# Optimization experiments

Measured on AMD Instinct MI355X. Metric: run time of the kernel, lower is better.

## Reference

```python
import jax, jax.numpy as jnp
import numpy as np

D = 1024      # d_model
E = 8         # num_experts
K = 2         # top_k
H = 4096      # expert_dim (bottleneck)
P = 256       # proj_dim
BATCH, SEQ = 2, 2048
CLAMP_MAX = float(np.log(1.0 / 0.01))
INIT_T = 0.5


def setup_inputs() -> dict:
    key = jax.random.key(0)
    ks = jax.random.split(key, 6)
    x = jax.random.normal(ks[0], (BATCH, SEQ, D), jnp.float32)
    # cosine projector (nn.Linear default init ~ U(-1/sqrt(D), 1/sqrt(D)))
    lim = 1.0 / np.sqrt(D)
    Wp = jax.random.uniform(ks[1], (P, D), jnp.float32, -lim, lim)
    bp = jnp.zeros((P,), jnp.float32)
    sim = 0.01 * jax.random.normal(ks[2], (P, E), jnp.float32)
    temp = jnp.full((1,), np.log(1.0 / INIT_T), jnp.float32)
    # RepAdapter 1x1 convs == linear layers; xavier_uniform, zero bias
    bA = float(np.sqrt(6.0 / (D + H)))
    A = jax.random.uniform(ks[3], (E, H, D), jnp.float32, -bA, bA)
    a_bias = jnp.zeros((E, H), jnp.float32)
    Bw = jax.random.uniform(ks[4], (E, D, H), jnp.float32, -bA, bA)
    b_bias = jnp.zeros((E, D), jnp.float32)
    return dict(x=x, Wp=Wp, bp=bp, sim=sim, temp=temp, A=A, a_bias=a_bias, Bw=Bw, b_bias=b_bias)


def reference(x, Wp, bp, sim, temp, A, a_bias, Bw, b_bias):
    B, S, d = x.shape
    e = sim.shape[1]
    xf = x.reshape(-1, d)                                  # [T, D]
    # cosine gate
    proj = xf @ Wp.T + bp                                  # [T, P]
    projn = proj / jnp.maximum(jnp.linalg.norm(proj, axis=1, keepdims=True), 1e-12)
    simn = sim / jnp.maximum(jnp.linalg.norm(sim, axis=0, keepdims=True), 1e-12)
    scale = jnp.exp(jnp.minimum(temp, CLAMP_MAX))          # [1]
    gate_probs = jax.nn.softmax((projn @ simn) * scale, axis=-1)   # [T, E]
    topv, topi = jax.lax.top_k(gate_probs, K)              # [T, K]
    topv = topv / (topv.sum(axis=-1, keepdims=True) + 1e-8)
    # per-token per-expert combine weight
    w = jnp.sum(topv[:, :, None] * jax.nn.one_hot(topi, e, dtype=x.dtype), axis=1)  # [T, E]

    # experts: y_e(x) = x + B_e(A_e x + a_e) + b_e (no nonlinearity); combine weighted
    def body(acc, params):
        Ae, ab, Be, bb, we = params
        h = xf @ Ae.T + ab                                 # [T, H]
        f = h @ Be.T + bb                                  # [T, D]
        return acc + we[:, None] * (xf + f), None

    out, _ = jax.lax.scan(body, jnp.zeros_like(xf), (A, a_bias, Bw, b_bias, w.T))
    out = out.reshape(B, S, d)

    frac = gate_probs.mean(axis=0)                         # expert_fractions
    aux_loss = jnp.sum((frac - 1.0 / e) ** 2)
    usage = jnp.bincount(topi.reshape(-1), length=e).astype(jnp.float32)
    return out, aux_loss, frac, usage
```

## Files before the change

kernel.cpp:

```cpp
#include <hip/hip_runtime.h>
#include <stdint.h>


typedef __attribute__((ext_vector_type(4))) float floatx4;
typedef __attribute__((ext_vector_type(8))) short shortx8;
typedef unsigned short ushort_t;

#define T_TOKENS 4096
#define D_DIM    1024
#define E_EXP    8
#define H_DIM    4096
#define P_DIM    256
#define ROWS_PAD 9344
#define MBLK     73

__device__ __forceinline__ ushort_t f2bf(float f) {
  union { float f; unsigned int u; } c; c.f = f;
  unsigned int u = c.u;
  unsigned int r = u + 0x7FFFu + ((u >> 16) & 1u);
  return (ushort_t)(r >> 16);
}

__global__ __launch_bounds__(256) void k_cvt(const float* __restrict__ src,
                                             ushort_t* __restrict__ dst, int n4) {
  int g = blockIdx.x * 256 + threadIdx.x;
  if (g >= n4) return;
  floatx4 v = ((const floatx4*)src)[g];
  ushort4 o; o.x = f2bf(v.x); o.y = f2bf(v.y); o.z = f2bf(v.z); o.w = f2bf(v.w);
  ((ushort4*)dst)[g] = o;
}

__global__ __launch_bounds__(256) void k_small_init(int* counts, int* cursor,
                                                    float* frac_sum, int* row2tok) {
  int g = blockIdx.x * 256 + threadIdx.x;
  if (g < 8) { counts[g] = 0; cursor[g] = 0; frac_sum[g] = 0.f; }
  if (g < ROWS_PAD) row2tok[g] = -1;
}

__global__ __launch_bounds__(256) void k_proj(const float* __restrict__ x,
                                              const float* __restrict__ Wp,
                                              const float* __restrict__ bp,
                                              float* __restrict__ proj) {
  __shared__ float Wc[256 * 36];
  __shared__ float Xc[16 * 36];
  int tid = threadIdx.x;
  int t0 = blockIdx.x * 16;
  int cg = tid & 31, tg = tid >> 5;
  floatx4 acc[2][8];
#pragma unroll
  for (int a = 0; a < 2; a++)
#pragma unroll
    for (int b = 0; b < 8; b++) acc[a][b] = (floatx4){0.f, 0.f, 0.f, 0.f};
  for (int kc = 0; kc < 32; ++kc) {
    int k0 = kc * 32;
    __syncthreads();
#pragma unroll
    for (int it = 0; it < 8; ++it) {
      int f = it * 256 + tid;
      int j = f >> 3, kk = (f & 7) << 2;
      floatx4 v = *(const floatx4*)(Wp + j * 1024 + k0 + kk);
      *(floatx4*)(Wc + j * 36 + kk) = v;
    }
    if (tid < 128) {
      int t = tid >> 3, kk = (tid & 7) << 2;
      floatx4 v = *(const floatx4*)(x + (size_t)(t0 + t) * 1024 + k0 + kk);
      *(floatx4*)(Xc + t * 36 + kk) = v;
    }
    __syncthreads();
#pragma unroll
    for (int k4 = 0; k4 < 8; ++k4) {
      floatx4 xv[2], wv[8];
#pragma unroll
      for (int tt = 0; tt < 2; tt++) xv[tt] = *(floatx4*)(Xc + (tg * 2 + tt) * 36 + k4 * 4);
#pragma unroll
      for (int jj = 0; jj < 8; jj++) wv[jj] = *(floatx4*)(Wc + (cg + jj * 32) * 36 + k4 * 4);
#pragma unroll
      for (int tt = 0; tt < 2; tt++)
#pragma unroll
        for (int jj = 0; jj < 8; jj++) acc[tt][jj] += xv[tt] * wv[jj];
    }
  }
#pragma unroll
  for (int tt = 0; tt < 2; tt++)
#pragma unroll
    for (int jj = 0; jj < 8; jj++) {
      floatx4 a = acc[tt][jj];
      float s = (a.x + a.y) + (a.z + a.w);
      int t = t0 + tg * 2 + tt, j = cg + jj * 32;
      proj[t * 256 + j] = s + bp[j];
    }
}

__global__ __launch_bounds__(128) void k_gate(const float* __restrict__ proj,
                                              const float* __restrict__ sim,
                                              const float* __restrict__ temp,
                                              int* __restrict__ topi, float* __restrict__ wslot,
                                              float* __restrict__ swsum,
                                              float* __restrict__ frac_sum, int* __restrict__ counts) {
  __shared__ float simT[8][256];
  __shared__ float snorm[8];
  __shared__ float fracs[8];
  __shared__ int cnts[8];
  int tid = threadIdx.x;
  for (int i = tid; i < 2048; i += 128) { int p = i >> 3, e = i & 7; simT[e][p] = sim[i]; }
  if (tid < 8) { fracs[tid] = 0.f; cnts[tid] = 0; }
  __syncthreads();
  if (tid < 8) {
    float s = 0.f;
    for (int p = 0; p < 256; p++) { float v = simT[tid][p]; s += v * v; }
    snorm[tid] = fmaxf(sqrtf(s), 1e-12f);
  }
  __syncthreads();
  int t = blockIdx.x * 128 + tid;
  floatx4 n4 = (floatx4){0.f, 0.f, 0.f, 0.f};
  floatx4 d4[8];
#pragma unroll
  for (int e = 0; e < 8; e++) d4[e] = (floatx4){0.f, 0.f, 0.f, 0.f};
  const floatx4* pr = (const floatx4*)(proj + t * 256);
  for (int k4 = 0; k4 < 64; ++k4) {
    floatx4 p = pr[k4];
    n4 += p * p;
#pragma unroll
    for (int e = 0; e < 8; e++) d4[e] += p * *(const floatx4*)(&simT[e][k4 * 4]);
  }
  float nrm = fmaxf(sqrtf((n4.x + n4.y) + (n4.z + n4.w)), 1e-12f);
  float scale = expf(fminf(temp[0], 4.6051701859880914f));
  float pe[8];
  float mx = -1e30f;
#pragma unroll
  for (int e = 0; e < 8; e++) {
    float d = (d4[e].x + d4[e].y) + (d4[e].z + d4[e].w);
    pe[e] = d / (nrm * snorm[e]) * scale;
    mx = fmaxf(mx, pe[e]);
  }
  float sum = 0.f;
#pragma unroll
  for (int e = 0; e < 8; e++) { pe[e] = expf(pe[e] - mx); sum += pe[e]; }
#pragma unroll
  for (int e = 0; e < 8; e++) pe[e] /= sum;
  int i0 = 0;
#pragma unroll
  for (int e = 1; e < 8; e++) if (pe[e] > pe[i0]) i0 = e;
  int i1 = (i0 == 0) ? 1 : 0;
#pragma unroll
  for (int e = 0; e < 8; e++) if (e != i1 && e != i0 && pe[e] > pe[i1]) i1 = e;
  float v0 = pe[i0], v1 = pe[i1];
  float s2 = v0 + v1 + 1e-8f;
  float w0 = v0 / s2, w1 = v1 / s2;
  topi[t * 2] = i0; topi[t * 2 + 1] = i1;
  wslot[t * 2] = w0; wslot[t * 2 + 1] = w1;
  swsum[t] = w0 + w1;
#pragma unroll
  for (int e = 0; e < 8; e++) atomicAdd(&fracs[e], pe[e]);
  atomicAdd(&cnts[i0], 1); atomicAdd(&cnts[i1], 1);
  __syncthreads();
  if (tid < 8) { atomicAdd(&frac_sum[tid], fracs[tid]); atomicAdd(&counts[tid], cnts[tid]); }
}

__global__ void k_scan(const int* __restrict__ counts, const float* __restrict__ frac_sum,
                       int* __restrict__ offsets, int* __restrict__ blk2e,
                       float* __restrict__ out_tail) {
  __shared__ int offs[9];
  if (threadIdx.x == 0) {
    int off = 0;
    for (int e = 0; e < 8; e++) { offs[e] = off; off += ((counts[e] + 127) >> 7) << 7; }
    offs[8] = off;
    for (int e = 0; e < 9; e++) offsets[e] = offs[e];
    float aux = 0.f;
    for (int e = 0; e < 8; e++) { float fr = frac_sum[e] / 4096.f; aux += (fr - 0.125f) * (fr - 0.125f); }
    out_tail[0] = aux;
  }
  __syncthreads();
  int tid = threadIdx.x;
  if (tid < MBLK) {
    int r = tid * 128, e = -1;
    for (int q = 0; q < 8; q++) if (r >= offs[q] && r < offs[q + 1]) e = q;
    blk2e[tid] = e;
  }
  if (tid < 8) {
    out_tail[1 + tid] = frac_sum[tid] / 4096.f;
    out_tail[9 + tid] = (float)counts[tid];
  }
}

__global__ __launch_bounds__(256) void k_assign(const int* __restrict__ topi,
                                                const float* __restrict__ wslot,
                                                const int* __restrict__ offsets,
                                                int* __restrict__ cursor,
                                                int* __restrict__ row2tok, float* __restrict__ roww) {
  int g = blockIdx.x * 256 + threadIdx.x;
  if (g >= 8192) return;
  int t = g >> 1;
  int e = topi[g];
  int pos = atomicAdd(&cursor[e], 1);
  int r = offsets[e] + pos;
  row2tok[r] = t;
  roww[r] = wslot[g];
}

__global__ __launch_bounds__(64) void k_gather(const float* __restrict__ x,
                                               const int* __restrict__ row2tok,
                                               ushort_t* __restrict__ xg) {
  int r = blockIdx.x;
  int t = row2tok[r];
  ushort4* dst = (ushort4*)(xg + (size_t)r * 1024);
  if (t < 0) {
    ushort4 z; z.x = z.y = z.z = z.w = 0;
    for (int i = threadIdx.x; i < 256; i += 64) dst[i] = z;
  } else {
    const floatx4* src = (const floatx4*)(x + (size_t)t * 1024);
    for (int i = threadIdx.x; i < 256; i += 64) {
      floatx4 v = src[i];
      ushort4 o; o.x = f2bf(v.x); o.y = f2bf(v.y); o.z = f2bf(v.z); o.w = f2bf(v.w);
      dst[i] = o;
    }
  }
}

__global__ __launch_bounds__(256) void k_init_out(const float* __restrict__ x,
                                                  const float* __restrict__ swsum,
                                                  float* __restrict__ out) {
  int g = blockIdx.x * 256 + threadIdx.x;
  float s = swsum[g >> 8];
  floatx4 v = ((const floatx4*)x)[g];
  ((floatx4*)out)[g] = v * s;
}

__global__ __launch_bounds__(256) void k_gemm(const ushort_t* __restrict__ Aop0,
                                              const ushort_t* __restrict__ Wall,
                                              const float* __restrict__ bias,
                                              const int* __restrict__ blk2e,
                                              int K, int N,
                                              ushort_t* __restrict__ hout,
                                              float* __restrict__ outp,
                                              const int* __restrict__ row2tok,
                                              const float* __restrict__ roww) {
  int e = blk2e[blockIdx.y];
  if (e < 0) return;
  int rb = blockIdx.y, nb = blockIdx.x;
  int Kslice = K / gridDim.z;
  int kbase = blockIdx.z * Kslice;
  const ushort_t* Aop = Aop0 + (size_t)rb * 128 * K + kbase;
  const ushort_t* Bop = Wall + (size_t)e * N * K + (size_t)nb * 128 * K + kbase;
  __shared__ ushort_t As[8192], Bs[8192];
  int tid = threadIdx.x, lane = tid & 63, wv = tid >> 6;
  int l15 = lane & 15, q = lane >> 4;
  int wm = (wv & 1) << 6, wn = (wv >> 1) << 6;
  floatx4 acc[4][4];
#pragma unroll
  for (int i = 0; i < 4; i++)
#pragma unroll
    for (int j = 0; j < 4; j++) acc[i][j] = (floatx4){0.f, 0.f, 0.f, 0.f};

  int row0 = tid >> 3, colc = tid & 7;
  size_t ga = (size_t)row0 * K + (size_t)(colc << 3);
  int wa = (row0 << 6) + ((colc ^ (row0 & 7)) << 3);
  int ksteps = Kslice >> 6;

  shortx8 rA[4], rB[4];
#pragma unroll
  for (int r = 0; r < 4; ++r) {
    rA[r] = *(const shortx8*)(Aop + ga + (size_t)(r * 32) * K);
    rB[r] = *(const shortx8*)(Bop + ga + (size_t)(r * 32) * K);
  }
  for (int ks = 0; ks < ksteps; ++ks) {
#pragma unroll
    for (int r = 0; r < 4; ++r) {
      *(shortx8*)(As + wa + r * 2048) = rA[r];
      *(shortx8*)(Bs + wa + r * 2048) = rB[r];
    }
    __syncthreads();
    int kn = (ks + 1 < ksteps) ? (ks + 1) : ks;
    const ushort_t* An = Aop + kn * 64;
    const ushort_t* Bn = Bop + kn * 64;
#pragma unroll
    for (int r = 0; r < 4; ++r) {
      rA[r] = *(const shortx8*)(An + ga + (size_t)(r * 32) * K);
      rB[r] = *(const shortx8*)(Bn + ga + (size_t)(r * 32) * K);
    }
#pragma unroll
    for (int s = 0; s < 2; ++s) {
      int cw = (s << 2) + q;
      shortx8 af[4], bfv[4];
#pragma unroll
      for (int i = 0; i < 4; i++) {
        int row = wm + i * 16 + l15;
        af[i] = *(const shortx8*)(As + (row << 6) + ((cw ^ (row & 7)) << 3));
      }
#pragma unroll
      for (int j = 0; j < 4; j++) {
        int row = wn + j * 16 + l15;
        bfv[j] = *(const shortx8*)(Bs + (row << 6) + ((cw ^ (row & 7)) << 3));
      }
#pragma unroll
      for (int i = 0; i < 4; i++)
#pragma unroll
        for (int j = 0; j < 4; j++)
          acc[i][j] = __builtin_amdgcn_mfma_f32_16x16x32_bf16(af[i], bfv[j], acc[i][j], 0, 0, 0);
    }
    __syncthreads();
  }
  const float* be = bias + (size_t)e * N + (size_t)nb * 128;
  if (hout) {
    ushort_t* hp = hout + (size_t)(rb * 128) * N + nb * 128;
#pragma unroll
    for (int j = 0; j < 4; j++) {
      int n = wn + j * 16 + l15;
      float bv = be[n];
#pragma unroll
      for (int i = 0; i < 4; i++)
#pragma unroll
        for (int r = 0; r < 4; r++) {
          int m = wm + i * 16 + (q << 2) + r;
          hp[(size_t)m * N + n] = f2bf(acc[i][j][r] + bv);
        }
    }
  } else {
    bool addb = (blockIdx.z == 0);
#pragma unroll
    for (int j = 0; j < 4; j++) {
      int n = wn + j * 16 + l15;
      float bv = addb ? be[n] : 0.f;
#pragma unroll
      for (int i = 0; i < 4; i++)
#pragma unroll
        for (int r = 0; r < 4; r++) {
          int m = wm + i * 16 + (q << 2) + r;
          int grow = rb * 128 + m;
          int tok = row2tok[grow];
          if (tok >= 0) {
            float v = (acc[i][j][r] + bv) * roww[grow];
            atomicAdd(outp + (size_t)tok * 1024 + nb * 128 + n, v);
          }
        }
    }
  }
}

extern "C" void kernel_launch(void* const* d_in, const int* in_sizes, int n_in,
                              void* d_out, int out_size, void* d_ws, size_t ws_size,
                              hipStream_t stream) {
  (void)in_sizes; (void)n_in; (void)out_size; (void)ws_size;
  const float* x      = (const float*)d_in[0];
  const float* Wp     = (const float*)d_in[1];
  const float* bp     = (const float*)d_in[2];
  const float* sim    = (const float*)d_in[3];
  const float* temp   = (const float*)d_in[4];
  const float* A      = (const float*)d_in[5];
  const float* a_bias = (const float*)d_in[6];
  const float* Bw     = (const float*)d_in[7];
  const float* b_bias = (const float*)d_in[8];
  float* out = (float*)d_out;

  char* ws = (char*)d_ws;
  ushort_t* Abf    = (ushort_t*)(ws);
  ushort_t* Bbf    = (ushort_t*)(ws + 67108864);
  ushort_t* xg     = (ushort_t*)(ws + 134217728);
  ushort_t* h      = (ushort_t*)(ws + 153354240);
  float*    proj   = (float*)   (ws + 229900288);
  int*      topi   = (int*)     (ws + 234094592);
  float*    wslot  = (float*)   (ws + 234127360);
  float*    swsum  = (float*)   (ws + 234160128);
  int*      row2tok= (int*)     (ws + 234176512);
  float*    roww   = (float*)   (ws + 234213888);
  int*      counts = (int*)     (ws + 234251264);
  int*      cursor = (int*)     (ws + 234251296);
  int*      offsets= (int*)     (ws + 234251328);
  int*      blk2e  = (int*)     (ws + 234251392);
  float*    fracs  = (float*)   (ws + 234251712);

  k_cvt<<<32768, 256, 0, stream>>>(A,  Abf, 8388608);
  k_cvt<<<32768, 256, 0, stream>>>(Bw, Bbf, 8388608);
  k_small_init<<<37, 256, 0, stream>>>(counts, cursor, fracs, row2tok);
  k_proj<<<256, 256, 0, stream>>>(x, Wp, bp, proj);
  k_gate<<<32, 128, 0, stream>>>(proj, sim, temp, topi, wslot, swsum, fracs, counts);
  k_scan<<<1, 128, 0, stream>>>(counts, fracs, offsets, blk2e, out + 4194304);
  k_assign<<<32, 256, 0, stream>>>(topi, wslot, offsets, cursor, row2tok, roww);
  k_gather<<<ROWS_PAD, 64, 0, stream>>>(x, row2tok, xg);
  k_init_out<<<4096, 256, 0, stream>>>(x, swsum, out);
  k_gemm<<<dim3(32, MBLK, 1), 256, 0, stream>>>(xg, Abf, a_bias, blk2e, 1024, 4096,
                                                h, nullptr, nullptr, nullptr);
  k_gemm<<<dim3(8, MBLK, 2), 256, 0, stream>>>(h, Bbf, b_bias, blk2e, 4096, 1024,
                                               nullptr, out, row2tok, roww);
}
```

Before: 802.1 us.

## Enlarge grouped GEMM tiles to 256x256 with direct-to-LDS double buffering

The grouped expert GEMM moves from 128x128 tiles with 256 threads to 256x256 tiles with 512 threads, and expert row blocks are padded to 256. Global-to-LDS staging now uses global_load_lds into double-buffered shared memory instead of going through registers, and the block index is remapped so neighbouring tiles land on the same XCD. The larger tiles are meant to raise arithmetic intensity and cut redundant weight traffic. The cost is more padding rows, fewer workgroups (risking underfill on the second GEMM), and higher register and LDS pressure.

```diff
diff --git a/kernel.cpp b/kernel.cpp
--- a/kernel.cpp
+++ b/kernel.cpp
@@ -11,14 +11,19 @@
 #define E_EXP    8
 #define H_DIM    4096
 #define P_DIM    256
-#define ROWS_PAD 9344
-#define MBLK     73
+#define ROWS_PAD 10240
+#define MBLK     40
 
 __device__ __forceinline__ ushort_t f2bf(float f) {
   union { float f; unsigned int u; } c; c.f = f;
   unsigned int u = c.u;
   unsigned int r = u + 0x7FFFu + ((u >> 16) & 1u);
   return (ushort_t)(r >> 16);
+}
+
+__device__ __forceinline__ void stage16(const ushort_t* g, ushort_t* l) {
+  __builtin_amdgcn_global_load_lds((const __attribute__((address_space(1))) void*)g,
+                                   (__attribute__((address_space(3))) void*)l, 16, 0, 0);
 }
 
 __global__ __launch_bounds__(256) void k_cvt(const float* __restrict__ src,
@@ -163,7 +168,7 @@
   __shared__ int offs[9];
   if (threadIdx.x == 0) {
     int off = 0;
-    for (int e = 0; e < 8; e++) { offs[e] = off; off += ((counts[e] + 127) >> 7) << 7; }
+    for (int e = 0; e < 8; e++) { offs[e] = off; off += ((counts[e] + 255) >> 8) << 8; }
     offs[8] = off;
     for (int e = 0; e < 9; e++) offsets[e] = offs[e];
     float aux = 0.f;
@@ -173,7 +178,7 @@
   __syncthreads();
   int tid = threadIdx.x;
   if (tid < MBLK) {
-    int r = tid * 128, e = -1;
+    int r = tid * 256, e = -1;
     for (int q = 0; q < 8; q++) if (r >= offs[q] && r < offs[q + 1]) e = q;
     blk2e[tid] = e;
   }
@@ -226,114 +231,135 @@
   ((floatx4*)out)[g] = v * s;
 }
 
-__global__ __launch_bounds__(256) void k_gemm(const ushort_t* __restrict__ Aop0,
-                                              const ushort_t* __restrict__ Wall,
-                                              const float* __restrict__ bias,
-                                              const int* __restrict__ blk2e,
-                                              int K, int N,
-                                              ushort_t* __restrict__ hout,
-                                              float* __restrict__ outp,
-                                              const int* __restrict__ row2tok,
-                                              const float* __restrict__ roww) {
-  int e = blk2e[blockIdx.y];
+__global__ __launch_bounds__(512, 2) void k_gemm(const ushort_t* __restrict__ Aop0,
+                                                 const ushort_t* __restrict__ Wall,
+                                                 const float* __restrict__ bias,
+                                                 const int* __restrict__ blk2e,
+                                                 int K, int N,
+                                                 ushort_t* __restrict__ hout,
+                                                 float* __restrict__ outp,
+                                                 const int* __restrict__ row2tok,
+                                                 const float* __restrict__ roww) {
+  int gx = gridDim.x;
+  int nwg = gx * gridDim.y;
+  int flat = blockIdx.y * gx + blockIdx.x;
+  int qq = nwg >> 3, rr = nwg & 7;
+  int xcd = flat & 7, idx = flat >> 3;
+  int swz = (xcd < rr ? xcd * (qq + 1) : rr * (qq + 1) + (xcd - rr) * qq) + idx;
+  int rb = swz / gx, nb = swz - rb * gx;
+
+  int e = blk2e[rb];
   if (e < 0) return;
-  int rb = blockIdx.y, nb = blockIdx.x;
   int Kslice = K / gridDim.z;
   int kbase = blockIdx.z * Kslice;
-  const ushort_t* Aop = Aop0 + (size_t)rb * 128 * K + kbase;
-  const ushort_t* Bop = Wall + (size_t)e * N * K + (size_t)nb * 128 * K + kbase;
-  __shared__ ushort_t As[8192], Bs[8192];
+  const ushort_t* Aop = Aop0 + (size_t)rb * 256 * K + kbase;
+  const ushort_t* Bop = Wall + (size_t)e * N * K + (size_t)nb * 256 * K + kbase;
+
+  __shared__ ushort_t As[2][256 * 64];
+  __shared__ ushort_t Bs[2][256 * 64];
+
   int tid = threadIdx.x, lane = tid & 63, wv = tid >> 6;
   int l15 = lane & 15, q = lane >> 4;
-  int wm = (wv & 1) << 6, wn = (wv >> 1) << 6;
-  floatx4 acc[4][4];
-#pragma unroll
-  for (int i = 0; i < 4; i++)
+  int wm = (wv >> 2) << 7;
+  int wn = (wv & 3) << 6;
+
+  floatx4 acc[8][4];
+#pragma unroll
+  for (int i = 0; i < 8; i++)
 #pragma unroll
     for (int j = 0; j < 4; j++) acc[i][j] = (floatx4){0.f, 0.f, 0.f, 0.f};
 
-  int row0 = tid >> 3, colc = tid & 7;
-  size_t ga = (size_t)row0 * K + (size_t)(colc << 3);
-  int wa = (row0 << 6) + ((colc ^ (row0 & 7)) << 3);
+  int srow = tid >> 3;
+  int scol = ((tid & 7) ^ (srow & 7)) << 3;
   int ksteps = Kslice >> 6;
-
-  shortx8 rA[4], rB[4];
-#pragma unroll
-  for (int r = 0; r < 4; ++r) {
-    rA[r] = *(const shortx8*)(Aop + ga + (size_t)(r * 32) * K);
-    rB[r] = *(const shortx8*)(Bop + ga + (size_t)(r * 32) * K);
-  }
+  int cur = 0;
+
+  {
+#pragma unroll
+    for (int r = 0; r < 4; ++r) {
+      int ldsoff = ((r << 9) + (wv << 6)) << 3;
+      size_t goff = (size_t)((r << 6) + srow) * K + scol;
+      stage16(Aop + goff, &As[0][ldsoff]);
+      stage16(Bop + goff, &Bs[0][ldsoff]);
+    }
+  }
+  __syncthreads();
+
   for (int ks = 0; ks < ksteps; ++ks) {
-#pragma unroll
-    for (int r = 0; r < 4; ++r) {
-      *(shortx8*)(As + wa + r * 2048) = rA[r];
-      *(shortx8*)(Bs + wa + r * 2048) = rB[r];
+    if (ks + 1 < ksteps) {
+      const ushort_t* An = Aop + (ks + 1) * 64;
+      const ushort_t* Bn = Bop + (ks + 1) * 64;
+      int nxt = cur ^ 1;
+#pragma unroll
+      for (int r = 0; r < 4; ++r) {
+        int ldsoff = ((r << 9) + (wv << 6)) << 3;
+        size_t goff = (size_t)((r << 6) + srow) * K + scol;
+        stage16(An + goff, &As[nxt][ldsoff]);
+        stage16(Bn + goff, &Bs[nxt][ldsoff]);
+      }
+    }
+    const ushort_t* Ab = As[cur];
+    const ushort_t* Bb = Bs[cur];
+#pragma unroll
+    for (int kc = 0; kc < 2; ++kc) {
+      int cw = (kc << 2) + q;
+      shortx8 af[8], bfv[4];
+#pragma unroll
+      for (int i = 0; i < 8; ++i) {
+        int row = wm + i * 16 + l15;
+        af[i] = *(const shortx8*)(Ab + (row << 6) + ((cw ^ (row & 7)) << 3));
+      }
+#pragma unroll
+      for (int j = 0; j < 4; ++j) {
+        int row = wn + j * 16 + l15;
+        bfv[j] = *(const shortx8*)(Bb + (row << 6) + ((cw ^ (row & 7)) << 3));
+      }
+#pragma unroll
+      for (int i = 0; i < 8; ++i)
+#pragma unroll
+        for (int j = 0; j < 4; ++j)
+          acc[i][j] = __builtin_amdgcn_mfma_f32_16x16x32_bf16(af[i], bfv[j], acc[i][j], 0, 0, 0);
     }
     __syncthreads();
-    int kn = (ks + 1 < ksteps) ? (ks + 1) : ks;
-    const ushort_t* An = Aop + kn * 64;
-    const ushort_t* Bn = Bop + kn * 64;
-#pragma unroll
-    for (int r = 0; r < 4; ++r) {
-      rA[r] = *(const shortx8*)(An + ga + (size_t)(r * 32) * K);
-      rB[r] = *(const shortx8*)(Bn + ga + (size_t)(r * 32) * K);
-    }
-#pragma unroll
-    for (int s = 0; s < 2; ++s) {
-      int cw = (s << 2) + q;
-      shortx8 af[4], bfv[4];
-#pragma unroll
-      for (int i = 0; i < 4; i++) {
-        int row = wm + i * 16 + l15;
-        af[i] = *(const shortx8*)(As + (row << 6) + ((cw ^ (row & 7)) << 3));
-      }
-#pragma unroll
-      for (int j = 0; j < 4; j++) {
-        int row = wn + j * 16 + l15;
-        bfv[j] = *(const shortx8*)(Bs + (row << 6) + ((cw ^ (row & 7)) << 3));
-      }
-#pragma unroll
-      for (int i = 0; i < 4; i++)
-#pragma unroll
-        for (int j = 0; j < 4; j++)
-          acc[i][j] = __builtin_amdgcn_mfma_f32_16x16x32_bf16(af[i], bfv[j], acc[i][j], 0, 0, 0);
-    }
-    __syncthreads();
-  }
-  const float* be = bias + (size_t)e * N + (size_t)nb * 128;
+    cur ^= 1;
+  }
+
+  const float* be = bias + (size_t)e * N + (size_t)nb * 256;
   if (hout) {
-    ushort_t* hp = hout + (size_t)(rb * 128) * N + nb * 128;
-#pragma unroll
-    for (int j = 0; j < 4; j++) {
+    ushort_t* hp = hout + (size_t)(rb * 256) * N + nb * 256;
+#pragma unroll
+    for (int j = 0; j < 4; ++j) {
       int n = wn + j * 16 + l15;
       float bv = be[n];
 #pragma unroll
-      for (int i = 0; i < 4; i++)
-#pragma unroll
-        for (int r = 0; r < 4; r++) {
+      for (int i = 0; i < 8; ++i)
+#pragma unroll
+        for (int r = 0; r < 4; ++r) {
           int m = wm + i * 16 + (q << 2) + r;
           hp[(size_t)m * N + n] = f2bf(acc[i][j][r] + bv);
         }
     }
   } else {
     bool addb = (blockIdx.z == 0);
-#pragma unroll
-    for (int j = 0; j < 4; j++) {
-      int n = wn + j * 16 + l15;
-      float bv = addb ? be[n] : 0.f;
-#pragma unroll
-      for (int i = 0; i < 4; i++)
-#pragma unroll
-        for (int r = 0; r < 4; r++) {
-          int m = wm + i * 16 + (q << 2) + r;
-          int grow = rb * 128 + m;
-          int tok = row2tok[grow];
-          if (tok >= 0) {
-            float v = (acc[i][j][r] + bv) * roww[grow];
-            atomicAdd(outp + (size_t)tok * 1024 + nb * 128 + n, v);
-          }
+    float bvv[4];
+#pragma unroll
+    for (int j = 0; j < 4; ++j) bvv[j] = addb ? be[wn + j * 16 + l15] : 0.f;
+#pragma unroll
+    for (int i = 0; i < 8; ++i)
+#pragma unroll
+      for (int r = 0; r < 4; ++r) {
+        int m = wm + i * 16 + (q << 2) + r;
+        int grow = rb * 256 + m;
+        int tok = row2tok[grow];
+        if (tok < 0) continue;
+        float w = roww[grow];
+        float* op = outp + (size_t)tok * 1024 + nb * 256;
+#pragma unroll
+        for (int j = 0; j < 4; ++j) {
+          int n = wn + j * 16 + l15;
+          atomicAdd(op + n, (acc[i][j][r] + bvv[j]) * w);
         }
-    }
+      }
   }
 }
 
@@ -356,30 +382,30 @@
   ushort_t* Abf    = (ushort_t*)(ws);
   ushort_t* Bbf    = (ushort_t*)(ws + 67108864);
   ushort_t* xg     = (ushort_t*)(ws + 134217728);
-  ushort_t* h      = (ushort_t*)(ws + 153354240);
-  float*    proj   = (float*)   (ws + 229900288);
-  int*      topi   = (int*)     (ws + 234094592);
-  float*    wslot  = (float*)   (ws + 234127360);
-  float*    swsum  = (float*)   (ws + 234160128);
-  int*      row2tok= (int*)     (ws + 234176512);
-  float*    roww   = (float*)   (ws + 234213888);
-  int*      counts = (int*)     (ws + 234251264);
-  int*      cursor = (int*)     (ws + 234251296);
-  int*      offsets= (int*)     (ws + 234251328);
-  int*      blk2e  = (int*)     (ws + 234251392);
-  float*    fracs  = (float*)   (ws + 234251712);
+  ushort_t* h      = (ushort_t*)(ws + 155189248);
+  float*    proj   = (float*)   (ws + 239075328);
+  int*      topi   = (int*)     (ws + 243269632);
+  float*    wslot  = (float*)   (ws + 243302400);
+  float*    swsum  = (float*)   (ws + 243335168);
+  int*      row2tok= (int*)     (ws + 243351552);
+  float*    roww   = (float*)   (ws + 243392512);
+  int*      counts = (int*)     (ws + 243433472);
+  int*      cursor = (int*)     (ws + 243433504);
+  int*      offsets= (int*)     (ws + 243433536);
+  int*      blk2e  = (int*)     (ws + 243433600);
+  float*    fracs  = (float*)   (ws + 243433760);
 
   k_cvt<<<32768, 256, 0, stream>>>(A,  Abf, 8388608);
   k_cvt<<<32768, 256, 0, stream>>>(Bw, Bbf, 8388608);
-  k_small_init<<<37, 256, 0, stream>>>(counts, cursor, fracs, row2tok);
+  k_small_init<<<40, 256, 0, stream>>>(counts, cursor, fracs, row2tok);
   k_proj<<<256, 256, 0, stream>>>(x, Wp, bp, proj);
   k_gate<<<32, 128, 0, stream>>>(proj, sim, temp, topi, wslot, swsum, fracs, counts);
   k_scan<<<1, 128, 0, stream>>>(counts, fracs, offsets, blk2e, out + 4194304);
   k_assign<<<32, 256, 0, stream>>>(topi, wslot, offsets, cursor, row2tok, roww);
   k_gather<<<ROWS_PAD, 64, 0, stream>>>(x, row2tok, xg);
   k_init_out<<<4096, 256, 0, stream>>>(x, swsum, out);
-  k_gemm<<<dim3(32, MBLK, 1), 256, 0, stream>>>(xg, Abf, a_bias, blk2e, 1024, 4096,
+  k_gemm<<<dim3(16, MBLK, 1), 512, 0, stream>>>(xg, Abf, a_bias, blk2e, 1024, 4096,
                                                 h, nullptr, nullptr, nullptr);
-  k_gemm<<<dim3(8, MBLK, 2), 256, 0, stream>>>(h, Bbf, b_bias, blk2e, 4096, 1024,
+  k_gemm<<<dim3(4, MBLK, 2), 512, 0, stream>>>(h, Bbf, b_bias, blk2e, 4096, 1024,
                                                nullptr, out, row2tok, roww);
 }
```

New measurement: 797.7 us. Within noise of the previous version (-0.5%).
